# Optimization experiments

Measured on AMD Instinct MI355X. Metric: run time of the kernel, lower is better.

## Reference

```python
import jax, jax.numpy as jnp
import numpy as np

B, L = 2048, 4096


def setup_inputs() -> dict:
    key = jax.random.key(0)
    k1, k2, k3 = jax.random.split(key, 3)
    j = jax.random.normal(k1, (1,), dtype=jnp.float32)
    b = jax.random.normal(k2, (2,), dtype=jnp.float32)
    observations = jax.random.randint(k3, (B, L), 0, 2, dtype=jnp.int64)
    return {"j": j, "b": b, "observations": observations}


def reference(j, b, observations):
    dt = j.dtype
    values = jnp.array([-0.5, 0.5], dtype=dt)           # 2 latent states
    pairs = values[:, None] * values[None, :]            # [2,2] outer product
    psi = j * pairs                                      # pairwise max-plus potential [2,2]
    # unary potentials: phi[b_idx, i, s] = b[obs[b_idx, i]] * values[s]
    phi = b[observations][..., None] * values            # [B, L, 2]
    zeros2 = jnp.zeros((2,), dtype=dt)

    def step(msg, phi_i):
        # max-plus message update: max over source state s of phi[s] + psi[s,t] + msg[s]
        new = jnp.max(phi_i[:, None] + psi + msg[:, None], axis=0)
        return new, new

    def per_seq(phi_seq):  # phi_seq: [L, 2]
        # forward messages: column 0 is zeros, column i+1 is msg from step i (i = 0..L-2)
        _, f = jax.lax.scan(step, zeros2, phi_seq[:-1])
        fwd = jnp.concatenate([zeros2[None], f], axis=0)       # [L, 2]
        # backward messages: iterate i = L-1 down to 1; msg from step i lands at column i-1
        _, bk = jax.lax.scan(step, zeros2, phi_seq[:0:-1])
        bwd = jnp.concatenate([bk[::-1], zeros2[None]], axis=0)  # [L, 2]
        return (phi_seq + fwd + bwd).T                          # [2, L]

    return jax.vmap(per_seq)(phi)  # [B, 2, L]
```

## Files before the change

kernel.cpp:

```cpp
#include <hip/hip_runtime.h>
#include <math.h>

#define L_SEQ 4096
#define NT 512
#define CHUNK 8
#define NW (NT/64)

struct M2 { float a00, a01, a10, a11; };

__device__ __forceinline__ M2 mpc(const M2& A, const M2& B) {
  M2 C;
  C.a00 = fmaxf(A.a00 + B.a00, A.a01 + B.a10);
  C.a01 = fmaxf(A.a00 + B.a01, A.a01 + B.a11);
  C.a10 = fmaxf(A.a10 + B.a00, A.a11 + B.a10);
  C.a11 = fmaxf(A.a10 + B.a01, A.a11 + B.a11);
  return C;
}

__device__ __forceinline__ M2 ldm(const float4& v) { return M2{v.x, v.y, v.z, v.w}; }
__device__ __forceinline__ float4 stm(const M2& m) { return make_float4(m.a00, m.a01, m.a10, m.a11); }

__global__ __launch_bounds__(NT, 8) void chain_fb_kernel(
    const float* __restrict__ jp, const float* __restrict__ bp,
    const int* __restrict__ obs, float* __restrict__ out) {
  __shared__ float4 T4s[16];
  __shared__ float T8a[256], T8b[256], T8c[256], T8d[256];
  __shared__ float4 wtf[NW];
  __shared__ float4 wtb[NW];

  const int t = threadIdx.x;
  const int lane = t & 63;
  const int w = t >> 6;
  const long b = blockIdx.x;

  const float P   = 0.25f * jp[0];
  const float hb0 = 0.5f * bp[0];
  const float hb1 = 0.5f * bp[1];

  const int4* rowp = (const int4*)(obs + b * L_SEQ + (long)t * CHUNK);
  int4 q0 = rowp[0], q1 = rowp[1];

  if (t < 16) {
    float u0 = (t & 1) ? hb1 : hb0;
    M2 Tt{P - u0, -u0 - P, u0 - P, u0 + P};
    #pragma unroll
    for (int k = 1; k < 4; ++k) {
      float uk = ((t >> k) & 1) ? hb1 : hb0;
      M2 Ek{P - uk, -uk - P, uk - P, uk + P};
      Tt = mpc(Tt, Ek);
    }
    T4s[t] = stm(Tt);
  }
  __syncthreads();
  if (t < 256) {
    M2 M = mpc(ldm(T4s[t & 15]), ldm(T4s[(t >> 4) & 15]));
    T8a[t] = M.a00; T8b[t] = M.a01; T8c[t] = M.a10; T8d[t] = M.a11;
  }

  unsigned m = (unsigned)(q0.x & 1)       | (unsigned)(q0.y & 1) << 1 |
               (unsigned)(q0.z & 1) << 2  | (unsigned)(q0.w & 1) << 3 |
               (unsigned)(q1.x & 1) << 4  | (unsigned)(q1.y & 1) << 5 |
               (unsigned)(q1.z & 1) << 6  | (unsigned)(q1.w & 1) << 7;
  __syncthreads();

  const unsigned r = __brev(m) >> 24;
  M2 T{T8a[m], T8b[m], T8c[m], T8d[m]};
  M2 R{T8a[r], T8b[r], T8c[r], T8d[r]};

  #pragma unroll
  for (int off = 1; off < 64; off <<= 1) {
    M2 OF{__shfl_up(T.a00, off), __shfl_up(T.a01, off),
          __shfl_up(T.a10, off), __shfl_up(T.a11, off)};
    M2 OB{__shfl_down(R.a00, off), __shfl_down(R.a01, off),
          __shfl_down(R.a10, off), __shfl_down(R.a11, off)};
    if (lane >= off)      T = mpc(OF, T);
    if (lane < 64 - off)  R = mpc(OB, R);
  }
  if (lane == 63) wtf[w] = stm(T);
  if (lane == 0)  wtb[w] = stm(R);

  M2 EF{__shfl_up(T.a00, 1), __shfl_up(T.a01, 1),
        __shfl_up(T.a10, 1), __shfl_up(T.a11, 1)};
  M2 EB{__shfl_down(R.a00, 1), __shfl_down(R.a01, 1),
        __shfl_down(R.a10, 1), __shfl_down(R.a11, 1)};
  if (lane == 0)  { EF.a00 = 0.f; EF.a01 = -INFINITY; EF.a10 = -INFINITY; EF.a11 = 0.f; }
  if (lane == 63) { EB.a00 = 0.f; EB.a01 = -INFINITY; EB.a10 = -INFINITY; EB.a11 = 0.f; }

  __syncthreads();

  M2 GF = EF, GB = EB;
  for (int ww = w - 1; ww >= 0; --ww) GF = mpc(ldm(wtf[ww]), GF);
  for (int ww = w + 1; ww < NW; ++ww) GB = mpc(ldm(wtb[ww]), GB);
  float fm0 = fmaxf(GF.a00, GF.a10), fm1 = fmaxf(GF.a01, GF.a11);
  float bm0 = fmaxf(GB.a00, GB.a10), bm1 = fmaxf(GB.a01, GB.a11);

  float o0[CHUNK], o1[CHUNK];
  #pragma unroll
  for (int e = 0; e < CHUNK; ++e) {
    float u = ((m >> e) & 1) ? hb1 : hb0;
    float x = fm0 - u, y = fm1 + u;
    o0[e] = x; o1[e] = y;
    fm0 = fmaxf(x + P, y - P);
    fm1 = fmaxf(x - P, y + P);
  }
  #pragma unroll
  for (int e = CHUNK - 1; e >= 0; --e) {
    float u = ((m >> e) & 1) ? hb1 : hb0;
    o0[e] += bm0; o1[e] += bm1;
    float x = bm0 - u, y = bm1 + u;
    bm0 = fmaxf(x + P, y - P);
    bm1 = fmaxf(x - P, y + P);
  }

  const long base = (long)t * CHUNK;
  float* r0 = out + b * (2L * L_SEQ) + base;
  float* r1 = r0 + L_SEQ;
  ((float4*)r0)[0] = make_float4(o0[0], o0[1], o0[2], o0[3]);
  ((float4*)r0)[1] = make_float4(o0[4], o0[5], o0[6], o0[7]);
  ((float4*)r1)[0] = make_float4(o1[0], o1[1], o1[2], o1[3]);
  ((float4*)r1)[1] = make_float4(o1[4], o1[5], o1[6], o1[7]);
}

extern "C" void kernel_launch(void* const* d_in, const int* in_sizes, int n_in,
                              void* d_out, int out_size, void* d_ws, size_t ws_size,
                              hipStream_t stream) {
  const float* jp  = (const float*)d_in[0];
  const float* bp  = (const float*)d_in[1];
  const int*   obs = (const int*)d_in[2];
  float* out = (float*)d_out;
  const int B = in_sizes[2] / L_SEQ;
  chain_fb_kernel<<<B, NT, 0, stream>>>(jp, bp, obs, out);
}
```

Measured before the change: 25.38 us.

## Split each sequence across two 256-thread blocks exchanging boundary messages via workspace

Each sequence is now handled by two 256-thread blocks, each covering one half. The blocks swap their half-chain max-plus boundary messages through global memory using atomic writes and a spin-wait on a sentinel value. A memset before the launch sets the workspace to that sentinel. The intent is smaller blocks and better occupancy or scheduling, at the cost of an extra memset, atomics, and a cross-block spin-wait that can deadlock if a partner block is not co-resident.

```diff
diff --git a/kernel.cpp b/kernel.cpp
--- a/kernel.cpp
+++ b/kernel.cpp
@@ -2,9 +2,10 @@
 #include <math.h>
 
 #define L_SEQ 4096
-#define NT 512
+#define NT 256
 #define CHUNK 8
 #define NW (NT/64)
+#define HALF (NT*CHUNK)
 
 struct M2 { float a00, a01, a10, a11; };
 
@@ -17,27 +18,38 @@
   return C;
 }
 
+__device__ __forceinline__ void mapply(float m0, float m1, const M2& M,
+                                       float& r0, float& r1) {
+  r0 = fmaxf(m0 + M.a00, m1 + M.a10);
+  r1 = fmaxf(m0 + M.a01, m1 + M.a11);
+}
+
 __device__ __forceinline__ M2 ldm(const float4& v) { return M2{v.x, v.y, v.z, v.w}; }
 __device__ __forceinline__ float4 stm(const M2& m) { return make_float4(m.a00, m.a01, m.a10, m.a11); }
 
 __global__ __launch_bounds__(NT, 8) void chain_fb_kernel(
     const float* __restrict__ jp, const float* __restrict__ bp,
-    const int* __restrict__ obs, float* __restrict__ out) {
+    const int* __restrict__ obs, float* __restrict__ out,
+    float* __restrict__ ws) {
   __shared__ float4 T4s[16];
   __shared__ float T8a[256], T8b[256], T8c[256], T8d[256];
   __shared__ float4 wtf[NW];
   __shared__ float4 wtb[NW];
+  __shared__ float vin_s[2];
 
   const int t = threadIdx.x;
   const int lane = t & 63;
   const int w = t >> 6;
-  const long b = blockIdx.x;
+  const int blk = blockIdx.x;
+  const int half = blk & 1;
+  const long seq = blk >> 1;
+  const int partner = blk ^ 1;
 
   const float P   = 0.25f * jp[0];
   const float hb0 = 0.5f * bp[0];
   const float hb1 = 0.5f * bp[1];
 
-  const int4* rowp = (const int4*)(obs + b * L_SEQ + (long)t * CHUNK);
+  const int4* rowp = (const int4*)(obs + seq * L_SEQ + half * HALF + (long)t * CHUNK);
   int4 q0 = rowp[0], q1 = rowp[1];
 
   if (t < 16) {
@@ -52,15 +64,15 @@
     T4s[t] = stm(Tt);
   }
   __syncthreads();
-  if (t < 256) {
+  {
     M2 M = mpc(ldm(T4s[t & 15]), ldm(T4s[(t >> 4) & 15]));
     T8a[t] = M.a00; T8b[t] = M.a01; T8c[t] = M.a10; T8d[t] = M.a11;
   }
-
-  unsigned m = (unsigned)(q0.x & 1)       | (unsigned)(q0.y & 1) << 1 |
-               (unsigned)(q0.z & 1) << 2  | (unsigned)(q0.w & 1) << 3 |
-               (unsigned)(q1.x & 1) << 4  | (unsigned)(q1.y & 1) << 5 |
-               (unsigned)(q1.z & 1) << 6  | (unsigned)(q1.w & 1) << 7;
+  const unsigned m =
+      (unsigned)(q0.x & 1)       | (unsigned)(q0.y & 1) << 1 |
+      (unsigned)(q0.z & 1) << 2  | (unsigned)(q0.w & 1) << 3 |
+      (unsigned)(q1.x & 1) << 4  | (unsigned)(q1.y & 1) << 5 |
+      (unsigned)(q1.z & 1) << 6  | (unsigned)(q1.w & 1) << 7;
   __syncthreads();
 
   const unsigned r = __brev(m) >> 24;
@@ -88,11 +100,36 @@
 
   __syncthreads();
 
+  if (t == 0) {
+    M2 tot;
+    if (half == 0)
+      tot = mpc(mpc(ldm(wtf[0]), ldm(wtf[1])), mpc(ldm(wtf[2]), ldm(wtf[3])));
+    else
+      tot = mpc(mpc(ldm(wtb[3]), ldm(wtb[2])), mpc(ldm(wtb[1]), ldm(wtb[0])));
+    atomicExch(&ws[2 * blk + 0], fmaxf(tot.a00, tot.a10));
+    atomicExch(&ws[2 * blk + 1], fmaxf(tot.a01, tot.a11));
+    float p0, p1;
+    do { p0 = atomicAdd(&ws[2 * partner + 0], 0.0f); }
+    while (__float_as_uint(p0) == 0xFFFFFFFFu);
+    do { p1 = atomicAdd(&ws[2 * partner + 1], 0.0f); }
+    while (__float_as_uint(p1) == 0xFFFFFFFFu);
+    vin_s[0] = p0; vin_s[1] = p1;
+  }
+
   M2 GF = EF, GB = EB;
   for (int ww = w - 1; ww >= 0; --ww) GF = mpc(ldm(wtf[ww]), GF);
   for (int ww = w + 1; ww < NW; ++ww) GB = mpc(ldm(wtb[ww]), GB);
-  float fm0 = fmaxf(GF.a00, GF.a10), fm1 = fmaxf(GF.a01, GF.a11);
-  float bm0 = fmaxf(GB.a00, GB.a10), bm1 = fmaxf(GB.a01, GB.a11);
+
+  __syncthreads();
+
+  float fm0, fm1, bm0, bm1;
+  if (half == 0) {
+    fm0 = fmaxf(GF.a00, GF.a10); fm1 = fmaxf(GF.a01, GF.a11);
+    mapply(vin_s[0], vin_s[1], GB, bm0, bm1);
+  } else {
+    mapply(vin_s[0], vin_s[1], GF, fm0, fm1);
+    bm0 = fmaxf(GB.a00, GB.a10); bm1 = fmaxf(GB.a01, GB.a11);
+  }
 
   float o0[CHUNK], o1[CHUNK];
   #pragma unroll
@@ -112,8 +149,8 @@
     bm1 = fmaxf(x - P, y + P);
   }
 
-  const long base = (long)t * CHUNK;
-  float* r0 = out + b * (2L * L_SEQ) + base;
+  const long base = (long)t * CHUNK + half * HALF;
+  float* r0 = out + seq * (2L * L_SEQ) + base;
   float* r1 = r0 + L_SEQ;
   ((float4*)r0)[0] = make_float4(o0[0], o0[1], o0[2], o0[3]);
   ((float4*)r0)[1] = make_float4(o0[4], o0[5], o0[6], o0[7]);
@@ -128,6 +165,9 @@
   const float* bp  = (const float*)d_in[1];
   const int*   obs = (const int*)d_in[2];
   float* out = (float*)d_out;
-  const int B = in_sizes[2] / L_SEQ;
-  chain_fb_kernel<<<B, NT, 0, stream>>>(jp, bp, obs, out);
+  float* ws  = (float*)d_ws;
+  const int B  = in_sizes[2] / L_SEQ;
+  const int nb = 2 * B;
+  hipMemsetAsync(ws, 0xFF, (size_t)nb * 2 * sizeof(float), stream);
+  chain_fb_kernel<<<nb, NT, 0, stream>>>(jp, bp, obs, out, ws);
 }
```

New measurement: 31.78 us. 25.2% more time.
